# Kernel optimization log

Measured on AMD Instinct MI355X. Metric: run time of the kernel, lower is better.

Reference implementation:

```python
import jax, jax.numpy as jnp
import numpy as np
from jax import lax

D_TEMPORAL, D_INNER, D_STATE, D_CONV, DT_RANK = 2, 4, 16, 4, 1
EPS = 1e-5


def setup_inputs() -> dict:
    key = jax.random.key(0)
    ks = jax.random.split(key, 14)
    B, L = 16, 32768
    f = lambda k, s, scale=1.0: jax.random.normal(k, s, jnp.float32) * scale
    dt_b = float(np.log(np.expm1(0.01)))  # softplus^-1(0.01), typical dt init
    A_log = jnp.log(jnp.tile(jnp.arange(1, D_STATE + 1, dtype=jnp.float32), (D_INNER, 1)))
    return {
        "hidden_states": f(ks[0], (B, D_TEMPORAL, L)),
        "norm_w": jnp.ones((D_TEMPORAL,), jnp.float32),
        "in_proj_w": f(ks[1], (2 * D_INNER, D_TEMPORAL), 0.5),
        "conv_w": f(ks[2], (D_INNER, D_CONV), 0.3),
        "conv_b": f(ks[3], (D_INNER,), 0.1),
        "x_proj_w": f(ks[4], (DT_RANK + 2 * D_STATE, D_INNER), 0.3),
        "dt_proj_w": f(ks[5], (D_INNER, DT_RANK), 1.0),
        "dt_proj_b": jnp.full((D_INNER,), dt_b, jnp.float32),
        "A_log": A_log,
        "D": jnp.ones((D_INNER,), jnp.float32),
        "conv_w_b": f(ks[6], (D_INNER, D_CONV), 0.3),
        "conv_b_b": f(ks[7], (D_INNER,), 0.1),
        "x_proj_w_b": f(ks[8], (DT_RANK + 2 * D_STATE, D_INNER), 0.3),
        "dt_proj_w_b": f(ks[9], (D_INNER, DT_RANK), 1.0),
        "dt_proj_b_b": jnp.full((D_INNER,), dt_b, jnp.float32),
        "A_b_log": A_log,
        "D_b": jnp.ones((D_INNER,), jnp.float32),
        "out_proj_w": f(ks[10], (D_TEMPORAL, D_INNER), 0.3),
        "norm_f_w": jnp.ones((D_TEMPORAL,), jnp.float32),
    }


def _silu(x):
    return x * jax.nn.sigmoid(x)


def _rmsnorm(x, w):
    return x * lax.rsqrt(jnp.mean(x * x, axis=-1, keepdims=True) + EPS) * w


def _branch(x, z, conv_w, conv_b, x_proj_w, dt_proj_w, dt_proj_b, A_log, D):
    # x, z: (B, d_inner, L). Causal depthwise conv + silu.
    Bb, d, L = x.shape
    xc = lax.conv_general_dilated(
        x, conv_w[:, None, :], (1,), [(D_CONV - 1, 0)],
        feature_group_count=d, dimension_numbers=("NCH", "OIH", "NCH"))
    u = _silu(xc + conv_b[None, :, None]).transpose(0, 2, 1)      # (B, L, d)
    x_dbl = u @ x_proj_w.T                                        # (B, L, rank+2n)
    dt, Bm, Cm = jnp.split(x_dbl, [DT_RANK, DT_RANK + D_STATE], axis=-1)
    dt = jax.nn.softplus(dt @ dt_proj_w.T + dt_proj_b)            # (B, L, d)
    A = -jnp.exp(A_log)                                           # (d, n)
    dA = jnp.exp(dt[..., None] * A)                               # (B, L, d, n)
    dBu = (dt * u)[..., None] * Bm[:, :, None, :]                 # (B, L, d, n)

    def step(h, inp):
        dA_t, dBu_t, C_t = inp
        h = dA_t * h + dBu_t                                      # (B, d, n)
        return h, jnp.einsum("bdn,bn->bd", h, C_t)

    h0 = jnp.zeros((Bb, d, D_STATE), dtype=u.dtype)
    _, ys = lax.scan(step, h0, (jnp.swapaxes(dA, 0, 1), jnp.swapaxes(dBu, 0, 1), jnp.swapaxes(Cm, 0, 1)))
    y = jnp.swapaxes(ys, 0, 1) + u * D                            # (B, L, d)
    return y * _silu(z.transpose(0, 2, 1))


def _forward(hidden_states, norm_w, in_proj_w, conv_w, conv_b, x_proj_w, dt_proj_w,
             dt_proj_b, A_log, D, conv_w_b, conv_b_b, x_proj_w_b, dt_proj_w_b,
             dt_proj_b_b, A_b_log, D_b, out_proj_w, norm_f_w):
    # hidden_states: (B, T=d_temporal, L); scan runs over L.
    hs = jnp.swapaxes(hidden_states, 1, 2)                        # (B, L, T)
    residual = hs.astype(jnp.float32)
    hs = _rmsnorm(residual, norm_w)
    xz = jnp.swapaxes(hs @ in_proj_w.T, 1, 2)                     # (B, 2*d_inner, L)
    x, z = jnp.split(xz, 2, axis=1)
    y_f = _branch(x, z, conv_w, conv_b, x_proj_w, dt_proj_w, dt_proj_b, A_log, D)
    y_b = _branch(x[..., ::-1], z[..., ::-1], conv_w_b, conv_b_b, x_proj_w_b,
                  dt_proj_w_b, dt_proj_b_b, A_b_log, D_b)
    y = y_f + y_b[:, ::-1, :]                                     # (B, L, d_inner)
    out = y @ out_proj_w.T                                        # (B, L, T)
    out = _rmsnorm(out + residual, norm_f_w)
    return jnp.swapaxes(out, 1, 2)                                # (B, T, L)


def reference(hidden_states, norm_w, in_proj_w, conv_w, conv_b, x_proj_w, dt_proj_w,
              dt_proj_b, A_log, D, conv_w_b, conv_b_b, x_proj_w_b, dt_proj_w_b,
              dt_proj_b_b, A_b_log, D_b, out_proj_w, norm_f_w):
    return _forward(hidden_states, norm_w, in_proj_w, conv_w, conv_b, x_proj_w,
                    dt_proj_w, dt_proj_b, A_log, D, conv_w_b, conv_b_b, x_proj_w_b,
                    dt_proj_w_b, dt_proj_b_b, A_b_log, D_b, out_proj_w, norm_f_w)
```

## Files before the change

### kernel.cpp

```cpp
#include <hip/hip_runtime.h>
#include <cstdint>

#define BB 16
#define LL 32768
#define NC 512
#define NSPAN 32
#define SPLEN 16
#define CPG 8

#define WD_SZ 256
#define XPW 0
#define CVW 132
#define CVB 148
#define DTW 152
#define DTB 156
#define AW  160
#define DW  224
#define G_INPROJ 512
#define G_NORMW 528
#define G_OUTP 530
#define G_NORMF 538
#define FLG 1000

#define PQ_OFF 4096
#define PQ_BYTES ((size_t)BB*2*NC*64*8)
#define SP_OFF (PQ_OFF + PQ_BYTES)
#define SP_BYTES ((size_t)BB*2*NSPAN*64*8)
#define SG_OFF (SP_OFF + SP_BYTES)
#define SG_BYTES ((size_t)BB*NC*2*64*4*4)
#define CG_OFF (SG_OFF + SG_BYTES)
#define CG_BYTES ((size_t)BB*NC*2*64*16*2)
#define YB_OFF (CG_OFF + CG_BYTES)
#define YB_BYTES ((size_t)BB*NC*64*4*4)

#define LOG2E 1.4426950408889634f

__device__ __forceinline__ float bf2f(unsigned short u){ return __uint_as_float(((unsigned int)u)<<16); }
__device__ __forceinline__ float blo(unsigned int u){ return __uint_as_float(u<<16); }
__device__ __forceinline__ float bhi(unsigned int u){ return __uint_as_float(u & 0xffff0000u); }

__device__ __forceinline__ unsigned int cvtpk(float lo, float hi){
  unsigned int r;
  asm("v_cvt_pk_bf16_f32 %0, %1, %2" : "=v"(r) : "v"(lo), "v"(hi));
  return r;
}
__device__ __forceinline__ unsigned short cvt1(float x){
  return (unsigned short)cvtpk(x, x);
}

__device__ __forceinline__ float siluf(float x){ return x / (1.f + __expf(-x)); }
__device__ __forceinline__ float softplusf_(float x){ return fmaxf(x,0.f) + log1pf(__expf(-fabsf(x))); }

__device__ __forceinline__ float exp2fast(float x){
#if __has_builtin(__builtin_amdgcn_exp2f)
  return __builtin_amdgcn_exp2f(x);
#else
  float r; asm("v_exp_f32 %0, %1\ns_nop 0" : "=v"(r) : "v"(x)); return r;
#endif
}

__device__ __forceinline__ float rowsum16(float x){
  asm("s_nop 1\n\t"
      "v_add_f32_dpp %0, %0, %0 row_ror:1 row_mask:0xf bank_mask:0xf\n\t"
      "s_nop 1\n\t"
      "v_add_f32_dpp %0, %0, %0 row_ror:2 row_mask:0xf bank_mask:0xf\n\t"
      "s_nop 1\n\t"
      "v_add_f32_dpp %0, %0, %0 row_ror:4 row_mask:0xf bank_mask:0xf\n\t"
      "s_nop 1\n\t"
      "v_add_f32_dpp %0, %0, %0 row_ror:8 row_mask:0xf bank_mask:0xf"
      : "+v"(x));
  return x;
}

__device__ __forceinline__ float wavescan_incl(float x){
  union { float f; int i; } a, t;
  a.f = x;
  t.i = __builtin_amdgcn_update_dpp(0, a.i, 0x111, 0xf, 0xf, true); a.f += t.f;
  t.i = __builtin_amdgcn_update_dpp(0, a.i, 0x112, 0xf, 0xf, true); a.f += t.f;
  t.i = __builtin_amdgcn_update_dpp(0, a.i, 0x114, 0xf, 0xf, true); a.f += t.f;
  t.i = __builtin_amdgcn_update_dpp(0, a.i, 0x118, 0xf, 0xf, true); a.f += t.f;
  t.i = __builtin_amdgcn_update_dpp(0, a.i, 0x142, 0xa, 0xf, true); a.f += t.f;
  t.i = __builtin_amdgcn_update_dpp(0, a.i, 0x143, 0xc, 0xf, true); a.f += t.f;
  return a.f;
}
__device__ __forceinline__ float readlane63(float x){
  union { float f; int i; } a; a.f = x;
  return __uint_as_float((unsigned)__builtin_amdgcn_readlane(a.i, 63));
}

__device__ __forceinline__ float ldw(const void* p, int i, int isf){
  return isf ? ((const float*)p)[i] : bf2f(((const unsigned short*)p)[i]);
}
__device__ __forceinline__ float2 hid2(const void* hid, int isf, int b, int t){
  if (isf){
    const float* p = (const float*)hid;
    return make_float2(p[(size_t)b*2*LL + t], p[(size_t)b*2*LL + LL + t]);
  }
  const unsigned short* p = (const unsigned short*)hid;
  return make_float2(bf2f(p[(size_t)b*2*LL + t]), bf2f(p[(size_t)b*2*LL + LL + t]));
}
__device__ __forceinline__ float4 xrow(const void* __restrict__ hid, int isf,
                                       const float* __restrict__ W, int b, int t){
  float2 h = hid2(hid, isf, b, t);
  float ms = rsqrtf(0.5f*(h.x*h.x + h.y*h.y) + 1e-5f);
  float v0 = h.x*ms*W[G_NORMW], v1 = h.y*ms*W[G_NORMW+1];
  float4 x;
  x.x = W[G_INPROJ+0]*v0 + W[G_INPROJ+1]*v1;
  x.y = W[G_INPROJ+2]*v0 + W[G_INPROJ+3]*v1;
  x.z = W[G_INPROJ+4]*v0 + W[G_INPROJ+5]*v1;
  x.w = W[G_INPROJ+6]*v0 + W[G_INPROJ+7]*v1;
  return x;
}

__global__ void k_prep(const void* __restrict__ normw, const void* __restrict__ inpj,
    const void* __restrict__ cwf, const void* __restrict__ cbf,
    const void* __restrict__ xpf, const void* __restrict__ dwf,
    const void* __restrict__ dbf, const void* __restrict__ alf,
    const void* __restrict__ ddf,
    const void* __restrict__ cwb, const void* __restrict__ cbb,
    const void* __restrict__ xpb, const void* __restrict__ dwb,
    const void* __restrict__ dbb, const void* __restrict__ alb,
    const void* __restrict__ ddb,
    const void* __restrict__ outp, const void* __restrict__ nfw,
    float* __restrict__ W)
{
  const int isf = (((const unsigned int*)ddf)[0] == 0x3F800000u) ? 1 : 0;
  int t = threadIdx.x;
  for (int i=t;i<132;i+=256){ W[XPW+i]=ldw(xpf,i,isf); W[WD_SZ+XPW+i]=ldw(xpb,i,isf); }
  for (int i=t;i<16;i+=256){ W[CVW+i]=ldw(cwf,i,isf); W[WD_SZ+CVW+i]=ldw(cwb,i,isf); W[G_INPROJ+i]=ldw(inpj,i,isf); }
  for (int i=t;i<4;i+=256){
    W[CVB+i]=ldw(cbf,i,isf); W[WD_SZ+CVB+i]=ldw(cbb,i,isf);
    W[DTW+i]=ldw(dwf,i,isf); W[WD_SZ+DTW+i]=ldw(dwb,i,isf);
    W[DTB+i]=ldw(dbf,i,isf); W[WD_SZ+DTB+i]=ldw(dbb,i,isf);
    W[DW+i] =ldw(ddf,i,isf); W[WD_SZ+DW+i] =ldw(ddb,i,isf);
  }
  for (int i=t;i<64;i+=256){
    W[AW+i]       = -__expf(ldw(alf,i,isf)) * LOG2E;
    W[WD_SZ+AW+i] = -__expf(ldw(alb,i,isf)) * LOG2E;
  }
  for (int i=t;i<8;i+=256) W[G_OUTP+i]=ldw(outp,i,isf);
  for (int i=t;i<2;i+=256){ W[G_NORMW+i]=ldw(normw,i,isf); W[G_NORMF+i]=ldw(nfw,i,isf); }
  if (t==0) W[FLG] = (float)isf;
}

template<int DR>
__device__ __forceinline__ float scan_local(const float (* __restrict__ dtPd)[68],
    const float (* __restrict__ dtud)[68],
    const unsigned int (* __restrict__ bcd)[68],
    float (* __restrict__ ySd)[68],
    float Ax, int d, int n)
{
  float h = 0.f;
  for (int j4=0; j4<16; j4++){
    const int t0 = DR ? 60-4*j4 : 4*j4;
    float4  d4 = *(const float4*)&dtPd[d][t0];
    float4  u4 = *(const float4*)&dtud[d][t0];
    uint4   c4 = *(const uint4*)&bcd[n][t0];
    float da[4]={d4.x,d4.y,d4.z,d4.w};
    float ua[4]={u4.x,u4.y,u4.z,u4.w};
    unsigned int ca[4]={c4.x,c4.y,c4.z,c4.w};
    float s[4];
    #pragma unroll
    for (int jr=0; jr<4; jr++){
      const int k  = DR ? 3-jr : jr;
      float e = exp2fast(Ax*da[k]);
      h = fmaf(e, h, ua[k]*blo(ca[k]));
      s[k] = rowsum16(h*bhi(ca[k]));
    }
    if (n == 0) *(float4*)&ySd[d][t0] = make_float4(s[0],s[1],s[2],s[3]);
  }
  return h;
}

__global__ __launch_bounds__(128, 4) void k_chunk2(const void* __restrict__ hid,
    const float* __restrict__ W, float2* __restrict__ PQ,
    float* __restrict__ sG, unsigned int* __restrict__ Cg,
    float4* __restrict__ YB)
{
  __shared__ __align__(16) char smx[2176];
  __shared__ __align__(16) float dtP[2][4][68];
  __shared__ __align__(16) float dtuP[2][4][68];
  __shared__ __align__(16) unsigned int BCp[2][16][68];
  __shared__ __align__(16) float uD[2][256];
  __shared__ float sTot[2][4];
  float4* xb = (float4*)smx;
  float (*yS)[4][68] = (float (*)[4][68])smx;

  const int tid  = threadIdx.x;
  const int wid  = tid >> 6;
  const int lane = tid & 63;
  const int gid  = blockIdx.x;
  const int c    = gid & (NC-1);
  const int b    = gid >> 9;
  const int isf  = (int)W[FLG];
  const size_t cd = (size_t)gid*2 + wid;

  if (tid < 70){
    int t2 = c*64 - 3 + tid;
    float4 v = make_float4(0.f,0.f,0.f,0.f);
    if (t2 >= 0 && t2 < LL) v = xrow(hid, isf, W, b, t2);
    xb[tid] = v;
  }
  __syncthreads();
  {
    const float* Wd = W + wid*WD_SZ;
    float4 a0,a1,a2,a3;
    if (wid == 0){ a0=xb[lane];   a1=xb[lane+1]; a2=xb[lane+2]; a3=xb[lane+3]; }
    else         { a0=xb[lane+6]; a1=xb[lane+5]; a2=xb[lane+4]; a3=xb[lane+3]; }
    float u[4];
    u[0] = siluf(Wd[CVB+0] + Wd[CVW+ 0]*a0.x + Wd[CVW+ 1]*a1.x + Wd[CVW+ 2]*a2.x + Wd[CVW+ 3]*a3.x);
    u[1] = siluf(Wd[CVB+1] + Wd[CVW+ 4]*a0.y + Wd[CVW+ 5]*a1.y + Wd[CVW+ 6]*a2.y + Wd[CVW+ 7]*a3.y);
    u[2] = siluf(Wd[CVB+2] + Wd[CVW+ 8]*a0.z + Wd[CVW+ 9]*a1.z + Wd[CVW+10]*a2.z + Wd[CVW+11]*a3.z);
    u[3] = siluf(Wd[CVB+3] + Wd[CVW+12]*a0.w + Wd[CVW+13]*a1.w + Wd[CVW+14]*a2.w + Wd[CVW+15]*a3.w);
    float dtr = Wd[XPW+0]*u[0] + Wd[XPW+1]*u[1] + Wd[XPW+2]*u[2] + Wd[XPW+3]*u[3];
    float4 ud4;
    #pragma unroll
    for (int d2=0; d2<4; d2++){
      float dt = softplusf_(fmaf(Wd[DTW+d2], dtr, Wd[DTB+d2]));
      dtP[wid][d2][lane]  = dt;
      dtuP[wid][d2][lane] = dt*u[d2];
      ((float*)&ud4)[d2] = u[d2]*Wd[DW+d2];
    }
    *(float4*)&uD[wid][lane*4] = ud4;
    float Cl[16];
    #pragma unroll
    for (int n=0; n<16; n++){
      float Bn = Wd[XPW+(1+n)*4+0]*u[0] + Wd[XPW+(1+n)*4+1]*u[1]
               + Wd[XPW+(1+n)*4+2]*u[2] + Wd[XPW+(1+n)*4+3]*u[3];
      float Cn = Wd[XPW+(17+n)*4+0]*u[0] + Wd[XPW+(17+n)*4+1]*u[1]
               + Wd[XPW+(17+n)*4+2]*u[2] + Wd[XPW+(17+n)*4+3]*u[3];
      BCp[wid][n][lane] = cvtpk(Bn, Cn);
      Cl[n] = Cn;
    }
    unsigned int cp[8];
    #pragma unroll
    for (int q=0;q<8;q++) cp[q] = cvtpk(Cl[2*q], Cl[2*q+1]);
    uint4* cgw = (uint4*)(Cg + cd*512);
    cgw[lane*2+0] = *(uint4*)&cp[0];
    cgw[lane*2+1] = *(uint4*)&cp[4];
  }
  __syncthreads();

  {
    float sv[4], tt[4];
    #pragma unroll
    for (int d2=0; d2<4; d2++){
      float v = dtP[wid][d2][lane];
      float x = wavescan_incl(v);
      float tot = readlane63(x);
      if (wid) x = tot - x + v;
      sv[d2] = x; tt[d2] = tot;
    }
    *(float4*)(sG + cd*256 + lane*4) = make_float4(sv[0],sv[1],sv[2],sv[3]);
    if (lane == 0){ sTot[wid][0]=tt[0]; sTot[wid][1]=tt[1]; sTot[wid][2]=tt[2]; sTot[wid][3]=tt[3]; }
  }

  const int d = lane>>4, n = lane&15;
  const float Ax = W[wid*WD_SZ + AW + d*16 + n];
  float h;
  size_t idx;
  if (wid == 0){
    h   = scan_local<0>(dtP[0], dtuP[0], BCp[0], yS[0], Ax, d, n);
    idx = ((size_t)(b*2+0)*NC + c);
  } else {
    h   = scan_local<1>(dtP[1], dtuP[1], BCp[1], yS[1], Ax, d, n);
    idx = ((size_t)(b*2+1)*NC + (NC-1-c));
  }
  float P = exp2fast(Ax * sTot[wid][d]);
  PQ[idx*64 + lane] = make_float2(P, h);
  __syncthreads();

  if (wid == 0){
    float4 v;
    v.x = yS[0][0][lane] + yS[1][0][lane] + uD[0][lane*4+0] + uD[1][lane*4+0];
    v.y = yS[0][1][lane] + yS[1][1][lane] + uD[0][lane*4+1] + uD[1][lane*4+1];
    v.z = yS[0][2][lane] + yS[1][2][lane] + uD[0][lane*4+2] + uD[1][lane*4+2];
    v.w = yS[0][3][lane] + yS[1][3][lane] + uD[0][lane*4+3] + uD[1][lane*4+3];
    YB[(size_t)gid*64 + lane] = v;
  }
}

__global__ __launch_bounds__(64) void k_spans(const float2* __restrict__ PQ,
                                              float2* __restrict__ SP)
{
  const int blk  = blockIdx.x;
  const int lane = threadIdx.x;
  const int bd   = blk >> 5, span = blk & (NSPAN-1);
  const float2* p = PQ + ((size_t)bd*NC + span*SPLEN)*64 + lane;
  float2 v[SPLEN];
  #pragma unroll
  for (int k=0;k<SPLEN;k++) v[k] = p[k*64];
  float A = 1.f, Bc = 0.f;
  #pragma unroll
  for (int k=0;k<SPLEN;k++){ A *= v[k].x; Bc = fmaf(v[k].x, Bc, v[k].y); }
  SP[((size_t)bd*NSPAN + span)*64 + lane] = make_float2(A,Bc);
}

__device__ __forceinline__ float compose_h0(const float2* __restrict__ PQ,
    const float2* __restrict__ SP, int bd, int p, int lane)
{
  const int s  = p >> 4, wn = p & 15;
  const float2* SPb = SP + (size_t)bd*NSPAN*64 + lane;
  const float2* PQb = PQ + ((size_t)bd*NC + (p & ~15))*64 + lane;
  float h = 0.f;
  #pragma unroll
  for (int jg=0; jg<4; jg++){
    if (jg*8 < s){
      float2 v[8];
      #pragma unroll
      for (int j=0;j<8;j++){ int jj = jg*8+j; v[j] = SPb[(size_t)(jj<s?jj:0)*64]; }
      #pragma unroll
      for (int j=0;j<8;j++){ int jj = jg*8+j; if (jj<s) h = fmaf(v[j].x, h, v[j].y); }
    }
  }
  #pragma unroll
  for (int jg=0; jg<2; jg++){
    if (jg*8 < wn){
      float2 v[8];
      #pragma unroll
      for (int j=0;j<8;j++){ int jj = jg*8+j; v[j] = PQb[(size_t)(jj<wn?jj:0)*64]; }
      #pragma unroll
      for (int j=0;j<8;j++){ int jj = jg*8+j; if (jj<wn) h = fmaf(v[j].x, h, v[j].y); }
    }
  }
  return h;
}

__global__ __launch_bounds__(128, 4) void k_final(const void* __restrict__ hid,
    const float* __restrict__ W, const float2* __restrict__ PQ,
    const float2* __restrict__ SP, const float* __restrict__ sG,
    const unsigned int* __restrict__ Cg, const float4* __restrict__ YB,
    void* __restrict__ out)
{
  __shared__ float h0s[2][64];
  __shared__ float As[2][64];
  __shared__ __align__(16) float4 yC[2][CPG][64];
  const int tid  = threadIdx.x;
  const int wid  = tid >> 6;
  const int lane = tid & 63;
  const int gb   = blockIdx.x;
  const int b    = gb >> 6;
  const int c0   = (gb & 63) * CPG;
  const int isf  = (int)W[FLG];
  const int bd   = b*2 + wid;

  As[wid][lane] = W[wid*WD_SZ + AW + lane];

  const int i_first = wid ? (CPG-1) : 0;
  const int c_first = c0 + i_first;
  const int p_first = wid ? (NC-1-c_first) : c_first;

  size_t cdf = ((size_t)(b*NC + c_first)*2 + wid);
  float4 s4 = *(const float4*)(sG + cdf*256 + lane*4);
  uint4 c8a = ((const uint4*)(Cg + cdf*512))[lane*2+0];
  uint4 c8b = ((const uint4*)(Cg + cdf*512))[lane*2+1];

  float h = compose_h0(PQ, SP, bd, p_first, lane);
  const float2* PQd = PQ + (size_t)bd*NC*64 + lane;

  for (int step=0; step<CPG; ++step){
    const int i_cur = wid ? (CPG-1-step) : step;
    const int c_cur = c0 + i_cur;
    const int hasN  = (step < CPG-1);

    float4 s4n; uint4 can, cbn;
    if (hasN){
      const int c_nxt = wid ? (c_cur-1) : (c_cur+1);
      size_t cdn = ((size_t)(b*NC + c_nxt)*2 + wid);
      s4n = *(const float4*)(sG + cdn*256 + lane*4);
      can = ((const uint4*)(Cg + cdn*512))[lane*2+0];
      cbn = ((const uint4*)(Cg + cdn*512))[lane*2+1];
    }

    h0s[wid][lane] = h;

    float cf[16];
    cf[ 0]=blo(c8a.x); cf[ 1]=bhi(c8a.x); cf[ 2]=blo(c8a.y); cf[ 3]=bhi(c8a.y);
    cf[ 4]=blo(c8a.z); cf[ 5]=bhi(c8a.z); cf[ 6]=blo(c8a.w); cf[ 7]=bhi(c8a.w);
    cf[ 8]=blo(c8b.x); cf[ 9]=bhi(c8b.x); cf[10]=blo(c8b.y); cf[11]=bhi(c8b.y);
    cf[12]=blo(c8b.z); cf[13]=bhi(c8b.z); cf[14]=blo(c8b.w); cf[15]=bhi(c8b.w);

    float4 cr;
    #pragma unroll
    for (int d2=0; d2<4; d2++){
      float sd = ((const float*)&s4)[d2];
      const float4* Af = (const float4*)&As[wid][d2*16];
      const float4* Hf = (const float4*)&h0s[wid][d2*16];
      float acc = 0.f;
      #pragma unroll
      for (int q=0;q<4;q++){
        float4 a4 = Af[q]; float4 h4 = Hf[q];
        acc = fmaf(exp2fast(a4.x*sd), cf[q*4+0]*h4.x, acc);
        acc = fmaf(exp2fast(a4.y*sd), cf[q*4+1]*h4.y, acc);
        acc = fmaf(exp2fast(a4.z*sd), cf[q*4+2]*h4.z, acc);
        acc = fmaf(exp2fast(a4.w*sd), cf[q*4+3]*h4.w, acc);
      }
      ((float*)&cr)[d2] = acc;
    }
    yC[wid][i_cur][lane] = cr;

    if (hasN){
      const int p_cur = wid ? (NC-1-c_cur) : c_cur;
      float2 pq = PQd[(size_t)p_cur*64];
      h = fmaf(pq.x, h, pq.y);
      s4 = s4n; c8a = can; c8b = cbn;
    }
  }
  __syncthreads();

  #pragma unroll
  for (int ii=0; ii<CPG/2; ii++){
    const int i  = wid*(CPG/2) + ii;
    const int c  = c0 + i;
    const int t  = lane;
    const int tg = c*64 + t;
    float4 cF = yC[0][i][t];
    float4 cB = yC[1][i][t];
    float4 yb = YB[(size_t)(b*NC + c)*64 + t];

    float2 r = hid2(hid, isf, b, tg);
    float ms0 = rsqrtf(0.5f*(r.x*r.x + r.y*r.y) + 1e-5f);
    float v0 = r.x*ms0*W[G_NORMW], v1 = r.y*ms0*W[G_NORMW+1];
    float z0 = siluf(W[G_INPROJ+ 8]*v0 + W[G_INPROJ+ 9]*v1);
    float z1 = siluf(W[G_INPROJ+10]*v0 + W[G_INPROJ+11]*v1);
    float z2 = siluf(W[G_INPROJ+12]*v0 + W[G_INPROJ+13]*v1);
    float z3 = siluf(W[G_INPROJ+14]*v0 + W[G_INPROJ+15]*v1);

    float y0 = (yb.x + cF.x + cB.x) * z0;
    float y1 = (yb.y + cF.y + cB.y) * z1;
    float y2 = (yb.z + cF.z + cB.z) * z2;
    float y3 = (yb.w + cF.w + cB.w) * z3;
    float o0 = W[G_OUTP+0]*y0 + W[G_OUTP+1]*y1 + W[G_OUTP+2]*y2 + W[G_OUTP+3]*y3;
    float o1 = W[G_OUTP+4]*y0 + W[G_OUTP+5]*y1 + W[G_OUTP+6]*y2 + W[G_OUTP+7]*y3;
    o0 += r.x;
    o1 += r.y;
    float ms = rsqrtf(0.5f*(o0*o0 + o1*o1) + 1e-5f);
    float e0 = o0*ms*W[G_NORMF], e1 = o1*ms*W[G_NORMF+1];
    size_t i0 = (size_t)b*2*LL + tg, i1 = i0 + LL;
    if (isf){
      ((float*)out)[i0] = e0;
      ((float*)out)[i1] = e1;
    } else {
      ((unsigned short*)out)[i0] = cvt1(e0);
      ((unsigned short*)out)[i1] = cvt1(e1);
    }
  }
}

extern "C" void kernel_launch(void* const* d_in, const int* in_sizes, int n_in,
                              void* d_out, int out_size, void* d_ws, size_t ws_size,
                              hipStream_t stream)
{
  (void)in_sizes; (void)n_in; (void)out_size; (void)ws_size;
  const void* hid   = d_in[0];
  const void* normw = d_in[1];
  const void* inpj  = d_in[2];
  const void* cwf   = d_in[3];
  const void* cbf   = d_in[4];
  const void* xpf   = d_in[5];
  const void* dwf   = d_in[6];
  const void* dbf   = d_in[7];
  const void* alf   = d_in[8];
  const void* ddf   = d_in[9];
  const void* cwb   = d_in[10];
  const void* cbb   = d_in[11];
  const void* xpb   = d_in[12];
  const void* dwb   = d_in[13];
  const void* dbb   = d_in[14];
  const void* alb   = d_in[15];
  const void* ddb   = d_in[16];
  const void* outp  = d_in[17];
  const void* nfw   = d_in[18];

  float* W            = (float*)d_ws;
  float2* PQ          = (float2*)((char*)d_ws + PQ_OFF);
  float2* SPt         = (float2*)((char*)d_ws + SP_OFF);
  float* sG           = (float*)((char*)d_ws + SG_OFF);
  unsigned int* Cg    = (unsigned int*)((char*)d_ws + CG_OFF);
  float4* YB          = (float4*)((char*)d_ws + YB_OFF);

  k_prep<<<1,256,0,stream>>>(normw, inpj, cwf, cbf, xpf, dwf, dbf, alf, ddf,
                             cwb, cbb, xpb, dwb, dbb, alb, ddb, outp, nfw, W);
  k_chunk2<<<BB*NC, 128, 0, stream>>>(hid, W, PQ, sG, Cg, YB);
  k_spans<<<BB*2*NSPAN, 64, 0, stream>>>(PQ, SPt);
  k_final<<<BB*(NC/CPG), 128, 0, stream>>>(hid, W, PQ, SPt, sG, Cg, YB, d_out);
}
```

Before: 185.1 us.

## Process one chunk per wave in k_final, composing both directions' h0 directly

k_final no longer walks 8 consecutive chunks per wave, carrying the forward and backward state through each step. Each wave now handles a single chunk. It composes the forward and backward initial states independently via compose_h0 and computes both corrections in one loop. This removes the serial per-step recurrence and the shared-memory staging of corrections, which gives much more parallelism. The cost is calling compose_h0 twice per chunk, which means more global loads of span and PQ prefixes in place of one composition per 8 chunks.

New measurement: 170.6 us. -7.8%, faster.

```diff
diff --git a/kernel.cpp b/kernel.cpp
--- a/kernel.cpp
+++ b/kernel.cpp
@@ -6,7 +6,6 @@
 #define NC 512
 #define NSPAN 32
 #define SPLEN 16
-#define CPG 8
 
 #define WD_SZ 256
 #define XPW 0
@@ -326,99 +325,72 @@
   return h;
 }
 
-__global__ __launch_bounds__(128, 4) void k_final(const void* __restrict__ hid,
+__global__ __launch_bounds__(256, 4) void k_final(const void* __restrict__ hid,
     const float* __restrict__ W, const float2* __restrict__ PQ,
     const float2* __restrict__ SP, const float* __restrict__ sG,
     const unsigned int* __restrict__ Cg, const float4* __restrict__ YB,
     void* __restrict__ out)
 {
-  __shared__ float h0s[2][64];
-  __shared__ float As[2][64];
-  __shared__ __align__(16) float4 yC[2][CPG][64];
-  const int tid  = threadIdx.x;
-  const int wid  = tid >> 6;
-  const int lane = tid & 63;
-  const int gb   = blockIdx.x;
-  const int b    = gb >> 6;
-  const int c0   = (gb & 63) * CPG;
+  __shared__ float h0sF[4][64];
+  __shared__ float h0sB[4][64];
+  const int lane = threadIdx.x & 63;
+  const int w    = threadIdx.x >> 6;
+  const int unit = blockIdx.x*4 + w;
+  const int b    = unit >> 9;
+  const int c    = unit & (NC-1);
   const int isf  = (int)W[FLG];
-  const int bd   = b*2 + wid;
-
-  As[wid][lane] = W[wid*WD_SZ + AW + lane];
-
-  const int i_first = wid ? (CPG-1) : 0;
-  const int c_first = c0 + i_first;
-  const int p_first = wid ? (NC-1-c_first) : c_first;
-
-  size_t cdf = ((size_t)(b*NC + c_first)*2 + wid);
-  float4 s4 = *(const float4*)(sG + cdf*256 + lane*4);
-  uint4 c8a = ((const uint4*)(Cg + cdf*512))[lane*2+0];
-  uint4 c8b = ((const uint4*)(Cg + cdf*512))[lane*2+1];
-
-  float h = compose_h0(PQ, SP, bd, p_first, lane);
-  const float2* PQd = PQ + (size_t)bd*NC*64 + lane;
-
-  for (int step=0; step<CPG; ++step){
-    const int i_cur = wid ? (CPG-1-step) : step;
-    const int c_cur = c0 + i_cur;
-    const int hasN  = (step < CPG-1);
-
-    float4 s4n; uint4 can, cbn;
-    if (hasN){
-      const int c_nxt = wid ? (c_cur-1) : (c_cur+1);
-      size_t cdn = ((size_t)(b*NC + c_nxt)*2 + wid);
-      s4n = *(const float4*)(sG + cdn*256 + lane*4);
-      can = ((const uint4*)(Cg + cdn*512))[lane*2+0];
-      cbn = ((const uint4*)(Cg + cdn*512))[lane*2+1];
-    }
-
-    h0s[wid][lane] = h;
-
-    float cf[16];
-    cf[ 0]=blo(c8a.x); cf[ 1]=bhi(c8a.x); cf[ 2]=blo(c8a.y); cf[ 3]=bhi(c8a.y);
-    cf[ 4]=blo(c8a.z); cf[ 5]=bhi(c8a.z); cf[ 6]=blo(c8a.w); cf[ 7]=bhi(c8a.w);
-    cf[ 8]=blo(c8b.x); cf[ 9]=bhi(c8b.x); cf[10]=blo(c8b.y); cf[11]=bhi(c8b.y);
-    cf[12]=blo(c8b.z); cf[13]=bhi(c8b.z); cf[14]=blo(c8b.w); cf[15]=bhi(c8b.w);
-
-    float4 cr;
-    #pragma unroll
-    for (int d2=0; d2<4; d2++){
-      float sd = ((const float*)&s4)[d2];
-      const float4* Af = (const float4*)&As[wid][d2*16];
-      const float4* Hf = (const float4*)&h0s[wid][d2*16];
-      float acc = 0.f;
-      #pragma unroll
-      for (int q=0;q<4;q++){
-        float4 a4 = Af[q]; float4 h4 = Hf[q];
-        acc = fmaf(exp2fast(a4.x*sd), cf[q*4+0]*h4.x, acc);
-        acc = fmaf(exp2fast(a4.y*sd), cf[q*4+1]*h4.y, acc);
-        acc = fmaf(exp2fast(a4.z*sd), cf[q*4+2]*h4.z, acc);
-        acc = fmaf(exp2fast(a4.w*sd), cf[q*4+3]*h4.w, acc);
-      }
-      ((float*)&cr)[d2] = acc;
-    }
-    yC[wid][i_cur][lane] = cr;
-
-    if (hasN){
-      const int p_cur = wid ? (NC-1-c_cur) : c_cur;
-      float2 pq = PQd[(size_t)p_cur*64];
-      h = fmaf(pq.x, h, pq.y);
-      s4 = s4n; c8a = can; c8b = cbn;
-    }
-  }
-  __syncthreads();
-
+
+  const size_t cdF = (size_t)unit*2, cdB = cdF + 1;
+  float4 sF = *(const float4*)(sG + cdF*256 + lane*4);
+  float4 sB = *(const float4*)(sG + cdB*256 + lane*4);
+  uint4 cFa = ((const uint4*)(Cg + cdF*512))[lane*2+0];
+  uint4 cFb = ((const uint4*)(Cg + cdF*512))[lane*2+1];
+  uint4 cBa = ((const uint4*)(Cg + cdB*512))[lane*2+0];
+  uint4 cBb = ((const uint4*)(Cg + cdB*512))[lane*2+1];
+  float4 yb = YB[(size_t)unit*64 + lane];
+  const int tg = c*64 + lane;
+  float2 r = hid2(hid, isf, b, tg);
+
+  float hF = compose_h0(PQ, SP, b*2+0, c,      lane);
+  float hB = compose_h0(PQ, SP, b*2+1, NC-1-c, lane);
+  h0sF[w][lane] = hF;
+  h0sB[w][lane] = hB;
+
+  float cfF[16], cfB[16];
+  cfF[ 0]=blo(cFa.x); cfF[ 1]=bhi(cFa.x); cfF[ 2]=blo(cFa.y); cfF[ 3]=bhi(cFa.y);
+  cfF[ 4]=blo(cFa.z); cfF[ 5]=bhi(cFa.z); cfF[ 6]=blo(cFa.w); cfF[ 7]=bhi(cFa.w);
+  cfF[ 8]=blo(cFb.x); cfF[ 9]=bhi(cFb.x); cfF[10]=blo(cFb.y); cfF[11]=bhi(cFb.y);
+  cfF[12]=blo(cFb.z); cfF[13]=bhi(cFb.z); cfF[14]=blo(cFb.w); cfF[15]=bhi(cFb.w);
+  cfB[ 0]=blo(cBa.x); cfB[ 1]=bhi(cBa.x); cfB[ 2]=blo(cBa.y); cfB[ 3]=bhi(cBa.y);
+  cfB[ 4]=blo(cBa.z); cfB[ 5]=bhi(cBa.z); cfB[ 6]=blo(cBa.w); cfB[ 7]=bhi(cBa.w);
+  cfB[ 8]=blo(cBb.x); cfB[ 9]=bhi(cBb.x); cfB[10]=blo(cBb.y); cfB[11]=bhi(cBb.y);
+  cfB[12]=blo(cBb.z); cfB[13]=bhi(cBb.z); cfB[14]=blo(cBb.w); cfB[15]=bhi(cBb.w);
+
+  float4 corr;
   #pragma unroll
-  for (int ii=0; ii<CPG/2; ii++){
-    const int i  = wid*(CPG/2) + ii;
-    const int c  = c0 + i;
-    const int t  = lane;
-    const int tg = c*64 + t;
-    float4 cF = yC[0][i][t];
-    float4 cB = yC[1][i][t];
-    float4 yb = YB[(size_t)(b*NC + c)*64 + t];
-
-    float2 r = hid2(hid, isf, b, tg);
+  for (int d2=0; d2<4; d2++){
+    float sdF = ((const float*)&sF)[d2];
+    float sdB = ((const float*)&sB)[d2];
+    float acc = 0.f;
+    #pragma unroll
+    for (int q=0;q<4;q++){
+      float4 aF = *(const float4*)(W + AW + d2*16 + q*4);
+      float4 aB = *(const float4*)(W + WD_SZ + AW + d2*16 + q*4);
+      float4 hF4 = *(const float4*)&h0sF[w][d2*16 + q*4];
+      float4 hB4 = *(const float4*)&h0sB[w][d2*16 + q*4];
+      acc = fmaf(exp2fast(aF.x*sdF), cfF[q*4+0]*hF4.x, acc);
+      acc = fmaf(exp2fast(aF.y*sdF), cfF[q*4+1]*hF4.y, acc);
+      acc = fmaf(exp2fast(aF.z*sdF), cfF[q*4+2]*hF4.z, acc);
+      acc = fmaf(exp2fast(aF.w*sdF), cfF[q*4+3]*hF4.w, acc);
+      acc = fmaf(exp2fast(aB.x*sdB), cfB[q*4+0]*hB4.x, acc);
+      acc = fmaf(exp2fast(aB.y*sdB), cfB[q*4+1]*hB4.y, acc);
+      acc = fmaf(exp2fast(aB.z*sdB), cfB[q*4+2]*hB4.z, acc);
+      acc = fmaf(exp2fast(aB.w*sdB), cfB[q*4+3]*hB4.w, acc);
+    }
+    ((float*)&corr)[d2] = acc;
+  }
+
+  {
     float ms0 = rsqrtf(0.5f*(r.x*r.x + r.y*r.y) + 1e-5f);
     float v0 = r.x*ms0*W[G_NORMW], v1 = r.y*ms0*W[G_NORMW+1];
     float z0 = siluf(W[G_INPROJ+ 8]*v0 + W[G_INPROJ+ 9]*v1);
@@ -426,10 +398,10 @@
     float z2 = siluf(W[G_INPROJ+12]*v0 + W[G_INPROJ+13]*v1);
     float z3 = siluf(W[G_INPROJ+14]*v0 + W[G_INPROJ+15]*v1);
 
-    float y0 = (yb.x + cF.x + cB.x) * z0;
-    float y1 = (yb.y + cF.y + cB.y) * z1;
-    float y2 = (yb.z + cF.z + cB.z) * z2;
-    float y3 = (yb.w + cF.w + cB.w) * z3;
+    float y0 = (yb.x + corr.x) * z0;
+    float y1 = (yb.y + corr.y) * z1;
+    float y2 = (yb.z + corr.z) * z2;
+    float y3 = (yb.w + corr.w) * z3;
     float o0 = W[G_OUTP+0]*y0 + W[G_OUTP+1]*y1 + W[G_OUTP+2]*y2 + W[G_OUTP+3]*y3;
     float o1 = W[G_OUTP+4]*y0 + W[G_OUTP+5]*y1 + W[G_OUTP+6]*y2 + W[G_OUTP+7]*y3;
     o0 += r.x;
@@ -483,5 +455,5 @@
                              cwb, cbb, xpb, dwb, dbb, alb, ddb, outp, nfw, W);
   k_chunk2<<<BB*NC, 128, 0, stream>>>(hid, W, PQ, sG, Cg, YB);
   k_spans<<<BB*2*NSPAN, 64, 0, stream>>>(PQ, SPt);
-  k_final<<<BB*(NC/CPG), 128, 0, stream>>>(hid, W, PQ, SPt, sG, Cg, YB, d_out);
-}
+  k_final<<<BB*NC/4, 256, 0, stream>>>(hid, W, PQ, SPt, sG, Cg, YB, d_out);
+}
```
